# Kernel optimization log

Hardware: AMD Instinct MI355X
Metric: run time of the kernel (lower is better)

The kernel has to match this reference:

```python
import jax, jax.numpy as jnp
import numpy as np

N = 8192
D = 256  # hidden_size = in_features = out_features
NEG_SLOPE = 0.01  # nn.LeakyReLU() default
MASK_VAL = -1e12


def setup_inputs() -> dict:
    key = jax.random.key(0)
    k1, k2, k3, k4 = jax.random.split(key, 4)
    x = jax.random.normal(k1, (N, D), dtype=jnp.float32)
    adj = jax.random.randint(k2, (N, N), 0, 2, dtype=jnp.int32)
    # kaiming_uniform_ style params (scaled random uniform)
    W = jax.random.normal(k3, (D, D), dtype=jnp.float32) * (1.0 / np.sqrt(D))
    a = jax.random.normal(k4, (2 * D, 1), dtype=jnp.float32) * (1.0 / np.sqrt(2 * D))
    return {"x": x, "adj": adj, "W": W, "a": a}


def reference(x, adj, W, a):
    # GraphAttentionLayer.forward (eval mode: dropout is identity)
    h = x @ W  # [N, D]
    # a_input[i,j] = concat(h_i, h_j); a_input @ a decomposes as:
    #   e[i,j] = h_i . a[:D] + h_j . a[D:]
    # identical math without materializing the [N, N, 2D] tensor.
    e_src = h @ a[:D, 0]  # [N]
    e_dst = h @ a[D:, 0]  # [N]
    e = e_src[:, None] + e_dst[None, :]  # [N, N]
    e = jnp.where(e > 0, e, NEG_SLOPE * e)  # LeakyReLU
    att_logits = jnp.where(adj > 0, e, MASK_VAL)
    attention = jax.nn.softmax(att_logits, axis=1)
    h_prime = attention @ h  # [N, D]
    return jax.nn.elu(h_prime)  # concat=True branch
```

## Files before the change

### kernel.cpp

```cpp
#include <hip/hip_runtime.h>

#define NN 8192
#define DD 256

typedef __attribute__((ext_vector_type(8))) short short8;
typedef __attribute__((ext_vector_type(4))) float f32x4;

__device__ __forceinline__ short f2bf(float x) {
    union { float f; unsigned u; } v; v.f = x;
    unsigned r = (v.u + 0x7FFFu + ((v.u >> 16) & 1u)) >> 16;
    return (short)r;
}
__device__ __forceinline__ float bf2f(short b) {
    union { float f; unsigned u; } v; v.u = ((unsigned)(unsigned short)b) << 16;
    return v.f;
}

__device__ __forceinline__ void barrier_keep_vmem() {
    asm volatile("s_waitcnt lgkmcnt(0)" ::: "memory");
    __builtin_amdgcn_s_barrier();
    asm volatile("" ::: "memory");
}

__global__ __launch_bounds__(256) void gat_pack(
    const int* __restrict__ adj, unsigned* __restrict__ bits)
{
    const int t   = threadIdx.x;
    const int row = blockIdx.x;
    const int* ar = adj + (size_t)row * NN;
    unsigned* br  = bits + (size_t)row * (NN / 32);
    #pragma unroll
    for (int i = 0; i < 8; ++i) {
        int j0 = i * 1024 + t * 4;
        int4 v = *(const int4*)(ar + j0);
        unsigned nib = (v.x > 0 ? 1u : 0u) | (v.y > 0 ? 2u : 0u)
                     | (v.z > 0 ? 4u : 0u) | (v.w > 0 ? 8u : 0u);
        unsigned word = nib << ((t & 7) * 4);
        word |= __shfl_xor((int)word, 1);
        word |= __shfl_xor((int)word, 2);
        word |= __shfl_xor((int)word, 4);
        if ((t & 7) == 0) br[i * 32 + (t >> 3)] = word;
    }
}

__global__ __launch_bounds__(256) void gat_prep(
    const float* __restrict__ x, const float* __restrict__ W,
    const float* __restrict__ a,
    short* __restrict__ hT, float* __restrict__ e_src, float* __restrict__ e_dst)
{
    __shared__ float x_s[32][260];
    __shared__ float W_s[2][16][256];
    const int t  = threadIdx.x;
    const int ib = blockIdx.x * 32;

    #pragma unroll
    for (int rep = 0; rep < 8; ++rep) {
        int fi = rep * 256 + t;
        int r  = fi >> 6;
        int c4 = (fi & 63) * 4;
        float4 v = *(const float4*)(x + (size_t)(ib + r) * DD + c4);
        *(float4*)&x_s[r][c4] = v;
    }
    float4 wp[4];
    #pragma unroll
    for (int q = 0; q < 4; ++q) {
        int fi = q * 256 + t;
        wp[q] = *(const float4*)(W + (size_t)(fi >> 6) * DD + (fi & 63) * 4);
    }
    barrier_keep_vmem();

    const int il = t >> 3;
    const int dg = (t & 7) * 4;
    f32x4 acc[8];
    #pragma unroll
    for (int m = 0; m < 8; ++m) acc[m] = (f32x4){0.f, 0.f, 0.f, 0.f};

    for (int kc = 0; kc < 16; ++kc) {
        const int b = kc & 1;
        #pragma unroll
        for (int q = 0; q < 4; ++q) {
            int fi = q * 256 + t;
            *(float4*)&W_s[b][fi >> 6][(fi & 63) * 4] = wp[q];
        }
        if (kc < 15) {
            #pragma unroll
            for (int q = 0; q < 4; ++q) {
                int fi = q * 256 + t;
                wp[q] = *(const float4*)(W + (size_t)((kc + 1) * 16 + (fi >> 6)) * DD + (fi & 63) * 4);
            }
        }
        barrier_keep_vmem();
        #pragma unroll
        for (int kl = 0; kl < 16; ++kl) {
            float xv = x_s[il][kc * 16 + kl];
            #pragma unroll
            for (int m = 0; m < 8; ++m) {
                float4 wv = *(const float4*)&W_s[b][kl][m * 32 + dg];
                acc[m].x += xv * wv.x; acc[m].y += xv * wv.y;
                acc[m].z += xv * wv.z; acc[m].w += xv * wv.w;
            }
        }
    }

    const int ig = ib + il;
    float p1 = 0.f, p2 = 0.f;
    #pragma unroll
    for (int m = 0; m < 8; ++m) {
        #pragma unroll
        for (int j = 0; j < 4; ++j) {
            int col = m * 32 + dg + j;
            float hv = acc[m][j];
            p1 += hv * a[col];
            p2 += hv * a[DD + col];
            hT[(size_t)col * NN + ig] = f2bf(hv);
        }
    }
    p1 += __shfl_xor(p1, 1); p1 += __shfl_xor(p1, 2); p1 += __shfl_xor(p1, 4);
    p2 += __shfl_xor(p2, 1); p2 += __shfl_xor(p2, 2); p2 += __shfl_xor(p2, 4);
    if ((t & 7) == 0) { e_src[ig] = p1; e_dst[ig] = p2; }
}

__global__ __launch_bounds__(512, 2) void gat_main(
    const unsigned* __restrict__ bits, const short* __restrict__ hT,
    const float* __restrict__ e_src, const float* __restrict__ e_dst,
    float* __restrict__ out)
{
    __shared__ float xch[8][32][132];
    __shared__ float denw[8][32];

    const int t    = threadIdx.x;
    const int lane = t & 63;
    const int w    = t >> 6;
    const int ibl  = blockIdx.x * 32;

    const int arow = lane & 15;
    const int kg8  = (lane >> 4) * 8;
    const int jw   = w * (NN / 8);

    const float es0 = e_src[ibl + arow];
    const float es1 = e_src[ibl + 16 + arow];
    const unsigned* br0 = bits + (size_t)(ibl + arow) * (NN / 32) + (jw >> 5);
    const unsigned* br1 = br0 + 16 * (NN / 32);
    const float* edp = e_dst + jw + kg8;
    const short* hB  = hT + (size_t)arow * NN + jw + kg8;

    f32x4 acc0[16], acc1[16];
    #pragma unroll
    for (int q = 0; q < 16; ++q) {
        acc0[q] = (f32x4){0.f, 0.f, 0.f, 0.f};
        acc1[q] = (f32x4){0.f, 0.f, 0.f, 0.f};
    }
    float dsum0 = 0.f, dsum1 = 0.f;

    #pragma unroll 2
    for (int n = 0; n < 32; ++n) {
        const int j32 = n * 32;
        unsigned bw0 = br0[n];
        unsigned bw1 = br1[n];
        float4 e0 = *(const float4*)(edp + j32);
        float4 e1 = *(const float4*)(edp + j32 + 4);
        int4 bq0[8], bq1[8];
        #pragma unroll
        for (int q = 0; q < 8; ++q)
            bq0[q] = *(const int4*)(hB + (size_t)q * 16 * NN + j32);

        short8 af0, af1;
        float ed[8] = {e0.x, e0.y, e0.z, e0.w, e1.x, e1.y, e1.z, e1.w};
        #pragma unroll
        for (int i = 0; i < 8; ++i) {
            float s0 = es0 + ed[i], s1 = es1 + ed[i];
            float l0 = s0 > 0.f ? s0 : 0.01f * s0;
            float l1 = s1 > 0.f ? s1 : 0.01f * s1;
            float w0 = ((bw0 >> (kg8 + i)) & 1u) ? __expf(l0) : 0.f;
            float w1 = ((bw1 >> (kg8 + i)) & 1u) ? __expf(l1) : 0.f;
            short b0 = f2bf(w0), b1 = f2bf(w1);
            af0[i] = b0; af1[i] = b1;
            dsum0 += bf2f(b0);
            dsum1 += bf2f(b1);
        }

        #pragma unroll
        for (int q = 0; q < 8; ++q)
            bq1[q] = *(const int4*)(hB + (size_t)(8 + q) * 16 * NN + j32);

        #pragma unroll
        for (int q = 0; q < 8; ++q) {
            acc0[q] = __builtin_amdgcn_mfma_f32_16x16x32_bf16(af0, *(short8*)&bq0[q], acc0[q], 0, 0, 0);
            acc1[q] = __builtin_amdgcn_mfma_f32_16x16x32_bf16(af1, *(short8*)&bq0[q], acc1[q], 0, 0, 0);
        }
        #pragma unroll
        for (int q = 0; q < 8; ++q) {
            acc0[8 + q] = __builtin_amdgcn_mfma_f32_16x16x32_bf16(af0, *(short8*)&bq1[q], acc0[8 + q], 0, 0, 0);
            acc1[8 + q] = __builtin_amdgcn_mfma_f32_16x16x32_bf16(af1, *(short8*)&bq1[q], acc1[8 + q], 0, 0, 0);
        }
    }

    dsum0 += __shfl_xor(dsum0, 16); dsum0 += __shfl_xor(dsum0, 32);
    dsum1 += __shfl_xor(dsum1, 16); dsum1 += __shfl_xor(dsum1, 32);
    if (lane < 16) { denw[w][lane] = dsum0; denw[w][16 + lane] = dsum1; }
    __syncthreads();

    const int ocol = lane & 15;
    const int orow = (lane >> 4) * 4;
    float inv[2][4];
    #pragma unroll
    for (int rh = 0; rh < 2; ++rh)
        #pragma unroll
        for (int i = 0; i < 4; ++i) {
            int row = rh * 16 + orow + i;
            float d = 0.f;
            #pragma unroll
            for (int sw = 0; sw < 8; ++sw) d += denw[sw][row];
            inv[rh][i] = 1.f / d;
        }

    #pragma unroll
    for (int p = 0; p < 2; ++p) {
        __syncthreads();
        #pragma unroll
        for (int q = 0; q < 8; ++q)
            #pragma unroll
            for (int i = 0; i < 4; ++i) {
                xch[w][orow + i][q * 16 + ocol]      = acc0[p * 8 + q][i];
                xch[w][16 + orow + i][q * 16 + ocol] = acc1[p * 8 + q][i];
            }
        __syncthreads();
        #pragma unroll
        for (int rh = 0; rh < 2; ++rh)
            #pragma unroll
            for (int i = 0; i < 4; ++i) {
                int row = rh * 16 + orow + i;
                float s = 0.f;
                #pragma unroll
                for (int sw = 0; sw < 8; ++sw) s += xch[sw][row][w * 16 + ocol];
                float v = s * inv[rh][i];
                v = v > 0.f ? v : expm1f(v);
                out[(size_t)(ibl + row) * DD + p * 128 + w * 16 + ocol] = v;
            }
    }
}

extern "C" void kernel_launch(void* const* d_in, const int* in_sizes, int n_in,
                              void* d_out, int out_size, void* d_ws, size_t ws_size,
                              hipStream_t stream) {
    const float* x   = (const float*)d_in[0];
    const int*   adj = (const int*)d_in[1];
    const float* W   = (const float*)d_in[2];
    const float* a   = (const float*)d_in[3];
    float* out = (float*)d_out;

    char* w0 = (char*)d_ws;
    short* hT      = (short*)w0;
    float* esrc    = (float*)(w0 + (size_t)DD * NN * 2);
    float* edst    = esrc + NN;
    unsigned* bits = (unsigned*)(edst + NN);

    gat_pack<<<dim3(NN), dim3(256), 0, stream>>>(adj, bits);
    gat_prep<<<dim3(NN / 32), dim3(256), 0, stream>>>(x, W, a, hT, esrc, edst);
    gat_main<<<dim3(NN / 32), dim3(512), 0, stream>>>(bits, hT, esrc, edst, out);
}
```

Measured before the change: 216.4 us.

## Split main kernel over column chunks with larger row tiles and separate reduction epilogue

The attention-matmul kernel now processes 256-row tiles split into 8 column (j) chunks, so each wave handles 64 rows by 128 output columns. This lets each loaded hT fragment feed four row tiles and raises reuse of the B operand. Partial numerators and denominators go to global workspace and a new epilogue kernel sums the partials, normalises and applies ELU. It also software-prefetches the next bitmask and e_dst values. In exchange it writes and rereads 8 partial [N,D] fp32 buffers (about 64MB each way) and adds a kernel launch.

```diff
diff --git a/kernel.cpp b/kernel.cpp
--- a/kernel.cpp
+++ b/kernel.cpp
@@ -2,6 +2,10 @@
 
 #define NN 8192
 #define DD 256
+#define BM 256
+#define JSPLIT 8
+#define JC (NN / JSPLIT)
+#define NT (JC / 32)
 
 typedef __attribute__((ext_vector_type(8))) short short8;
 typedef __attribute__((ext_vector_type(4))) float f32x4;
@@ -123,121 +127,122 @@
 __global__ __launch_bounds__(512, 2) void gat_main(
     const unsigned* __restrict__ bits, const short* __restrict__ hT,
     const float* __restrict__ e_src, const float* __restrict__ e_dst,
-    float* __restrict__ out)
-{
-    __shared__ float xch[8][32][132];
-    __shared__ float denw[8][32];
-
+    float* __restrict__ num, float* __restrict__ den_part)
+{
     const int t    = threadIdx.x;
     const int lane = t & 63;
     const int w    = t >> 6;
-    const int ibl  = blockIdx.x * 32;
-
+    const int jc   = blockIdx.x & (JSPLIT - 1);
+    const int rb   = blockIdx.x >> 3;
+    const int jbase = jc * JC;
+    const int rowq = w & 3;
+    const int colh = w >> 2;
     const int arow = lane & 15;
     const int kg8  = (lane >> 4) * 8;
-    const int jw   = w * (NN / 8);
-
-    const float es0 = e_src[ibl + arow];
-    const float es1 = e_src[ibl + 16 + arow];
-    const unsigned* br0 = bits + (size_t)(ibl + arow) * (NN / 32) + (jw >> 5);
-    const unsigned* br1 = br0 + 16 * (NN / 32);
-    const float* edp = e_dst + jw + kg8;
-    const short* hB  = hT + (size_t)arow * NN + jw + kg8;
-
-    f32x4 acc0[16], acc1[16];
-    #pragma unroll
-    for (int q = 0; q < 16; ++q) {
-        acc0[q] = (f32x4){0.f, 0.f, 0.f, 0.f};
-        acc1[q] = (f32x4){0.f, 0.f, 0.f, 0.f};
-    }
-    float dsum0 = 0.f, dsum1 = 0.f;
-
-    #pragma unroll 2
-    for (int n = 0; n < 32; ++n) {
+    const int rbase = rb * BM + rowq * 64;
+
+    float es[4];
+    const unsigned* brp[4];
+    #pragma unroll
+    for (int rt = 0; rt < 4; ++rt) {
+        es[rt]  = e_src[rbase + rt * 16 + arow];
+        brp[rt] = bits + (size_t)(rbase + rt * 16 + arow) * (NN / 32) + (jbase >> 5);
+    }
+    const float* edp = e_dst + jbase + kg8;
+    const short* hB  = hT + (size_t)(colh * 128 + arow) * NN + jbase + kg8;
+
+    f32x4 acc[4][8];
+    #pragma unroll
+    for (int rt = 0; rt < 4; ++rt)
+        #pragma unroll
+        for (int q = 0; q < 8; ++q) acc[rt][q] = (f32x4){0.f, 0.f, 0.f, 0.f};
+    float ds[4] = {0.f, 0.f, 0.f, 0.f};
+
+    unsigned bw[4];
+    #pragma unroll
+    for (int rt = 0; rt < 4; ++rt) bw[rt] = brp[rt][0];
+    float4 e0 = *(const float4*)(edp);
+    float4 e1 = *(const float4*)(edp + 4);
+
+    for (int n = 0; n < NT; ++n) {
         const int j32 = n * 32;
-        unsigned bw0 = br0[n];
-        unsigned bw1 = br1[n];
-        float4 e0 = *(const float4*)(edp + j32);
-        float4 e1 = *(const float4*)(edp + j32 + 4);
-        int4 bq0[8], bq1[8];
+        int4 bq[8];
         #pragma unroll
         for (int q = 0; q < 8; ++q)
-            bq0[q] = *(const int4*)(hB + (size_t)q * 16 * NN + j32);
-
-        short8 af0, af1;
+            bq[q] = *(const int4*)(hB + (size_t)q * 16 * NN + j32);
+
         float ed[8] = {e0.x, e0.y, e0.z, e0.w, e1.x, e1.y, e1.z, e1.w};
-        #pragma unroll
-        for (int i = 0; i < 8; ++i) {
-            float s0 = es0 + ed[i], s1 = es1 + ed[i];
-            float l0 = s0 > 0.f ? s0 : 0.01f * s0;
-            float l1 = s1 > 0.f ? s1 : 0.01f * s1;
-            float w0 = ((bw0 >> (kg8 + i)) & 1u) ? __expf(l0) : 0.f;
-            float w1 = ((bw1 >> (kg8 + i)) & 1u) ? __expf(l1) : 0.f;
-            short b0 = f2bf(w0), b1 = f2bf(w1);
-            af0[i] = b0; af1[i] = b1;
-            dsum0 += bf2f(b0);
-            dsum1 += bf2f(b1);
-        }
-
-        #pragma unroll
-        for (int q = 0; q < 8; ++q)
-            bq1[q] = *(const int4*)(hB + (size_t)(8 + q) * 16 * NN + j32);
-
+        short8 af[4];
+        #pragma unroll
+        for (int rt = 0; rt < 4; ++rt) {
+            #pragma unroll
+            for (int i = 0; i < 8; ++i) {
+                float s = es[rt] + ed[i];
+                float l = s > 0.f ? s : 0.01f * s;
+                float wv = ((bw[rt] >> (kg8 + i)) & 1u) ? __expf(l) : 0.f;
+                short b = f2bf(wv);
+                af[rt][i] = b;
+                ds[rt] += bf2f(b);
+            }
+        }
+        if (n + 1 < NT) {
+            #pragma unroll
+            for (int rt = 0; rt < 4; ++rt) bw[rt] = brp[rt][n + 1];
+            e0 = *(const float4*)(edp + j32 + 32);
+            e1 = *(const float4*)(edp + j32 + 36);
+        }
+        #pragma unroll
+        for (int rt = 0; rt < 4; ++rt)
+            #pragma unroll
+            for (int q = 0; q < 8; ++q)
+                acc[rt][q] = __builtin_amdgcn_mfma_f32_16x16x32_bf16(
+                    af[rt], *(short8*)&bq[q], acc[rt][q], 0, 0, 0);
+    }
+
+    #pragma unroll
+    for (int rt = 0; rt < 4; ++rt) {
+        float d = ds[rt];
+        d += __shfl_xor(d, 16);
+        d += __shfl_xor(d, 32);
+        if (colh == 0 && lane < 16)
+            den_part[(size_t)jc * NN + rbase + rt * 16 + lane] = d;
+    }
+
+    float* np = num + (size_t)jc * NN * DD;
+    const int r4 = (lane >> 4) * 4;
+    #pragma unroll
+    for (int rt = 0; rt < 4; ++rt)
         #pragma unroll
         for (int q = 0; q < 8; ++q) {
-            acc0[q] = __builtin_amdgcn_mfma_f32_16x16x32_bf16(af0, *(short8*)&bq0[q], acc0[q], 0, 0, 0);
-            acc1[q] = __builtin_amdgcn_mfma_f32_16x16x32_bf16(af1, *(short8*)&bq0[q], acc1[q], 0, 0, 0);
-        }
-        #pragma unroll
-        for (int q = 0; q < 8; ++q) {
-            acc0[8 + q] = __builtin_amdgcn_mfma_f32_16x16x32_bf16(af0, *(short8*)&bq1[q], acc0[8 + q], 0, 0, 0);
-            acc1[8 + q] = __builtin_amdgcn_mfma_f32_16x16x32_bf16(af1, *(short8*)&bq1[q], acc1[8 + q], 0, 0, 0);
-        }
-    }
-
-    dsum0 += __shfl_xor(dsum0, 16); dsum0 += __shfl_xor(dsum0, 32);
-    dsum1 += __shfl_xor(dsum1, 16); dsum1 += __shfl_xor(dsum1, 32);
-    if (lane < 16) { denw[w][lane] = dsum0; denw[w][16 + lane] = dsum1; }
-    __syncthreads();
-
-    const int ocol = lane & 15;
-    const int orow = (lane >> 4) * 4;
-    float inv[2][4];
-    #pragma unroll
-    for (int rh = 0; rh < 2; ++rh)
-        #pragma unroll
-        for (int i = 0; i < 4; ++i) {
-            int row = rh * 16 + orow + i;
-            float d = 0.f;
-            #pragma unroll
-            for (int sw = 0; sw < 8; ++sw) d += denw[sw][row];
-            inv[rh][i] = 1.f / d;
-        }
-
-    #pragma unroll
-    for (int p = 0; p < 2; ++p) {
-        __syncthreads();
-        #pragma unroll
-        for (int q = 0; q < 8; ++q)
-            #pragma unroll
-            for (int i = 0; i < 4; ++i) {
-                xch[w][orow + i][q * 16 + ocol]      = acc0[p * 8 + q][i];
-                xch[w][16 + orow + i][q * 16 + ocol] = acc1[p * 8 + q][i];
-            }
-        __syncthreads();
-        #pragma unroll
-        for (int rh = 0; rh < 2; ++rh)
-            #pragma unroll
-            for (int i = 0; i < 4; ++i) {
-                int row = rh * 16 + orow + i;
-                float s = 0.f;
-                #pragma unroll
-                for (int sw = 0; sw < 8; ++sw) s += xch[sw][row][w * 16 + ocol];
-                float v = s * inv[rh][i];
-                v = v > 0.f ? v : expm1f(v);
-                out[(size_t)(ibl + row) * DD + p * 128 + w * 16 + ocol] = v;
-            }
-    }
+            size_t o = (size_t)(rbase + rt * 16 + r4) * DD + colh * 128 + q * 16 + arow;
+            #pragma unroll
+            for (int r = 0; r < 4; ++r)
+                np[o + (size_t)r * DD] = acc[rt][q][r];
+        }
+}
+
+__global__ __launch_bounds__(256) void gat_epi(
+    float* __restrict__ out, const float* __restrict__ num,
+    const float* __restrict__ den_part)
+{
+    int idx = blockIdx.x * 256 + threadIdx.x;
+    int row = idx >> 6;
+    float d = 0.f;
+    #pragma unroll
+    for (int p = 0; p < JSPLIT; ++p) d += den_part[(size_t)p * NN + row];
+    float4 s = {0.f, 0.f, 0.f, 0.f};
+    #pragma unroll
+    for (int p = 0; p < JSPLIT; ++p) {
+        float4 v = ((const float4*)(num + (size_t)p * NN * DD))[idx];
+        s.x += v.x; s.y += v.y; s.z += v.z; s.w += v.w;
+    }
+    float inv = 1.f / d;
+    float4 o;
+    o.x = s.x * inv; o.x = o.x > 0.f ? o.x : expm1f(o.x);
+    o.y = s.y * inv; o.y = o.y > 0.f ? o.y : expm1f(o.y);
+    o.z = s.z * inv; o.z = o.z > 0.f ? o.z : expm1f(o.z);
+    o.w = s.w * inv; o.w = o.w > 0.f ? o.w : expm1f(o.w);
+    ((float4*)out)[idx] = o;
 }
 
 extern "C" void kernel_launch(void* const* d_in, const int* in_sizes, int n_in,
@@ -254,8 +259,12 @@
     float* esrc    = (float*)(w0 + (size_t)DD * NN * 2);
     float* edst    = esrc + NN;
     unsigned* bits = (unsigned*)(edst + NN);
+    float* den     = (float*)((char*)bits + (size_t)NN * (NN / 32) * 4);
+    float* num     = den + (size_t)JSPLIT * NN;
 
     gat_pack<<<dim3(NN), dim3(256), 0, stream>>>(adj, bits);
     gat_prep<<<dim3(NN / 32), dim3(256), 0, stream>>>(x, W, a, hT, esrc, edst);
-    gat_main<<<dim3(NN / 32), dim3(512), 0, stream>>>(bits, hT, esrc, edst, out);
-}
+    gat_main<<<dim3((NN / BM) * JSPLIT), dim3(512), 0, stream>>>(
+        bits, hT, esrc, edst, num, den);
+    gat_epi<<<dim3(NN * DD / 4 / 256), dim3(256), 0, stream>>>(out, num, den);
+}
```

New measurement: 211.4 us. 2.3% less time.
